# Kernel tuning notes

Hardware: AMD Instinct MI355X
Metric: run time of the kernel (lower is better)

## Reference

```python
import jax, jax.numpy as jnp
import numpy as np

B = 1024          # number of graphs
N = 64            # atoms per graph
NUM_NODES = B * N
HID = 256         # hidden_channels
H1 = HID // 2
E = 2_097_152     # edges (avg degree 32)


def _xavier(k, fan_in, fan_out):
    lim = np.sqrt(6.0 / (fan_in + fan_out)).astype(np.float32)
    return jax.random.uniform(k, (fan_in, fan_out), jnp.float32, -lim, lim)


def setup_inputs() -> dict:
    key = jax.random.key(0)
    ks = jax.random.split(key, 6)
    node_features = jax.random.normal(ks[0], (NUM_NODES, HID), jnp.float32)
    edge_index = jax.random.randint(ks[1], (2, E), 0, NUM_NODES)
    batch = jnp.repeat(jnp.arange(B), N)  # sorted graph ids, equal-size graphs
    W1 = _xavier(ks[2], HID + 1, H1); b1 = jnp.zeros((H1,), jnp.float32)
    W2 = _xavier(ks[3], H1, H1);      b2 = jnp.zeros((H1,), jnp.float32)
    W3 = _xavier(ks[4], H1, 1);       b3 = jnp.zeros((1,), jnp.float32)
    kT = jnp.ones((1,), jnp.float32)
    return {"node_features": node_features, "W1": W1, "b1": b1, "W2": W2,
            "b2": b2, "W3": W3, "b3": b3, "kT": kT,
            "edge_index": edge_index, "batch": batch}


def reference(node_features, W1, b1, W2, b2, W3, b3, kT, edge_index, batch):
    num_nodes = node_features.shape[0]
    # node degree: count of occurrences as source node
    deg = jnp.zeros((num_nodes,), jnp.float32).at[edge_index[0]].add(1.0)
    # per-graph atom counts and segment start offsets (n_atoms_i)
    counts = jax.ops.segment_sum(jnp.ones((num_nodes,), jnp.float32), batch,
                                 num_segments=B)
    start = jnp.cumsum(counts) - counts  # exclusive cumsum
    # stable per-graph sort of degrees in one shot: lexsort keys, primary=batch
    order = jnp.lexsort((deg, batch))  # global original indices, sorted by (batch, deg)
    # connectivity feature: local original index of the k-th smallest-degree
    # node in its graph, normalized by graph size (matches sorted_index / n_atoms_i)
    conn = (order.astype(jnp.float32) - start[batch]) / counts[batch]
    # MLP(hidden+1 -> hid/2 -> hid/2 -> 1) with silu
    x = jnp.concatenate([conn[:, None], node_features], axis=-1)  # [nodes, HID+1]
    h = jax.nn.silu(x @ W1 + b1)
    h = jax.nn.silu(h @ W2 + b2)
    logits = (h @ W3 + b3)[:, 0] / kT[0]
    # per-graph (segment) softmax
    m = jax.ops.segment_max(logits, batch, num_segments=B)
    e = jnp.exp(logits - m[batch])
    s = jax.ops.segment_sum(e, batch, num_segments=B)
    return e / s[batch]  # concat of per-graph softmaxed probabilities
```

## Files before the change

kernel.cpp:

```cpp
#include <hip/hip_runtime.h>

#define NB 1024
#define NPG 64
#define NUM_NODES 65536
#define HID 256
#define H1DIM 128
#define NE 2097152
#define GH 128

typedef __attribute__((ext_vector_type(8))) _Float16 f16x8;
typedef __attribute__((ext_vector_type(4))) float f32x4;

#define PART_OFF (128*1024)

__device__ __forceinline__ void dma16(const void* g, void* l) {
    __builtin_amdgcn_global_load_lds(
        (const __attribute__((address_space(1))) unsigned int*)g,
        (__attribute__((address_space(3))) unsigned int*)l, 16, 0, 0);
}

__global__ __launch_bounds__(256) void prep_hist_kernel(
    const float* __restrict__ W1, const float* __restrict__ W2,
    _Float16* __restrict__ wf,
    const int4* __restrict__ src4, unsigned int* __restrict__ partials)
{
    __shared__ unsigned int h[16384];
    const int bx = blockIdx.x;
    const int t = threadIdx.x;

    if (bx < 96) {
        const int L = t & 63;
        const int j2 = (t >> 6) * 2;
        const float* src;
        _Float16* dst;
        int kt, nt;
        if (bx < 64) { kt = bx >> 3; nt = bx & 7; src = W1 + H1DIM; dst = wf + bx * 512; }
        else { int bb = bx - 64; kt = bb >> 3; nt = bb & 7; src = W2; dst = wf + 32768 + bb * 512; }
        const int k = kt * 32 + (L >> 4) * 8 + j2;
        const int n = nt * 16 + (L & 15);
        dst[L * 8 + j2]     = (_Float16)src[k * H1DIM + n];
        dst[L * 8 + j2 + 1] = (_Float16)src[(k + 1) * H1DIM + n];
        return;
    }

    const int b = bx - 96;
    uint4* h4 = (uint4*)h;
#pragma unroll
    for (int i = 0; i < 16; ++i) h4[t + i * 256] = make_uint4(0u, 0u, 0u, 0u);
    __syncthreads();
    const int4* p = src4 + b * ((NE / 4) / GH);
#pragma unroll 4
    for (int i = t; i < (NE / 4) / GH; i += 256) {
        int4 v = p[i];
        atomicAdd(&h[v.x >> 2], 1u << ((v.x & 3) * 8));
        atomicAdd(&h[v.y >> 2], 1u << ((v.y & 3) * 8));
        atomicAdd(&h[v.z >> 2], 1u << ((v.z & 3) * 8));
        atomicAdd(&h[v.w >> 2], 1u << ((v.w & 3) * 8));
    }
    __syncthreads();
    uint4* dst = (uint4*)(partials + b * 16384);
#pragma unroll
    for (int i = 0; i < 16; ++i) dst[t + i * 256] = h4[t + i * 256];
}

__global__ __launch_bounds__(512, 4) void mlp_softmax_kernel(
    const float* __restrict__ feat,
    const float* __restrict__ W1, const float* __restrict__ b1,
    const float* __restrict__ b2,
    const float* __restrict__ W3, const float* __restrict__ b3,
    const float* __restrict__ kT,
    const _Float16* __restrict__ wf,
    const unsigned int* __restrict__ partials,
    float* __restrict__ out)
{
    __shared__ _Float16 wfs[32768];
    __shared__ unsigned int dpart[2][16][16];
    __shared__ unsigned int degs[2][NPG];
    __shared__ float conns[2][NPG];
    __shared__ float logits_s[2][NPG];

    const int tid = threadIdx.x;
    const int L = tid & 63;
    const int w = __builtin_amdgcn_readfirstlane(tid >> 6);
    const int h = w >> 2;
    const int w4 = w & 3;
    const int q = L >> 4;
    const int c = L & 15;
    const int g0 = blockIdx.x * 2;
    const int node0 = g0 * NPG;

#pragma unroll
    for (int i = 0; i < 8; ++i)
        dma16(&wf[(i * 512 + tid) * 8], &wfs[(i * 512 + w * 64) * 8]);

    {
        const int t256 = tid & 255;
        const int wd = t256 & 15, sg = t256 >> 4;
        const unsigned int* p = partials + (size_t)(sg * 8) * 16384 + (g0 + h) * 16 + wd;
        unsigned int s = 0;
#pragma unroll
        for (int i = 0; i < 8; ++i) s += p[(size_t)i * 16384];
        dpart[h][sg][wd] = s;
    }

    const float* featw = &feat[(size_t)(node0 + h * 64 + w4 * 16 + c) * HID + q * 8];
    float4 fa[8], fb[8];
#pragma unroll
    for (int kt = 0; kt < 8; ++kt) {
        fa[kt] = *(const float4*)(featw + kt * 32);
        fb[kt] = *(const float4*)(featw + kt * 32 + 4);
    }
    float b1v[8], w1r0[8];
#pragma unroll
    for (int nt = 0; nt < 8; ++nt) {
        b1v[nt]  = b1[nt * 16 + c];
        w1r0[nt] = W1[nt * 16 + c];
    }

    __syncthreads();
    if (tid < 32) {
        const int hh = tid >> 4, wd = tid & 15;
        unsigned int s = 0;
#pragma unroll
        for (int k = 0; k < 16; ++k) s += dpart[hh][k][wd];
        degs[hh][wd * 4 + 0] = s & 255u;
        degs[hh][wd * 4 + 1] = (s >> 8) & 255u;
        degs[hh][wd * 4 + 2] = (s >> 16) & 255u;
        degs[hh][wd * 4 + 3] = s >> 24;
    }
    __syncthreads();
    if ((tid & 192) == 0) {
        const int hh = tid >> 8, i = tid & 63;
        unsigned int di = degs[hh][i];
        int rk = 0;
#pragma unroll 8
        for (int j = 0; j < NPG; ++j) {
            unsigned int dj = degs[hh][j];
            rk += (int)((dj < di) | ((dj == di) & (j < i)));
        }
        conns[hh][rk] = (float)i * (1.0f / 64.0f);
    }
    __syncthreads();

    f16x8 af[8];
#pragma unroll
    for (int kt = 0; kt < 8; ++kt) {
        float4 A = fa[kt], B = fb[kt];
        f16x8 v = { (_Float16)A.x, (_Float16)A.y, (_Float16)A.z, (_Float16)A.w,
                    (_Float16)B.x, (_Float16)B.y, (_Float16)B.z, (_Float16)B.w };
        af[kt] = v;
    }

    float cn[4];
#pragma unroll
    for (int r = 0; r < 4; ++r) cn[r] = conns[h][w4 * 16 + q * 4 + r];
    f32x4 acc[8];
#pragma unroll
    for (int nt = 0; nt < 8; ++nt)
#pragma unroll
        for (int r = 0; r < 4; ++r)
            acc[nt][r] = fmaf(cn[r], w1r0[nt], b1v[nt]);

#pragma unroll
    for (int kt = 0; kt < 8; ++kt) {
#pragma unroll
        for (int nt = 0; nt < 8; ++nt) {
            f16x8 bfv = *(const f16x8*)&wfs[(kt * 8 + nt) * 512 + L * 8];
            acc[nt] = __builtin_amdgcn_mfma_f32_16x16x32_f16(af[kt], bfv, acc[nt], 0, 0, 0);
        }
    }

    __syncthreads();

#pragma unroll
    for (int i = 0; i < 4; ++i)
        dma16(&wf[32768 + (i * 512 + tid) * 8], &wfs[(i * 512 + w * 64) * 8]);

#pragma unroll
    for (int nt = 0; nt < 8; ++nt) {
        const int ktp = nt >> 1;
        const int lp = (((nt & 1) << 1) + (c >> 3)) * 16 + q * 4;
        const int j = c & 7;
#pragma unroll
        for (int r = 0; r < 4; ++r) {
            float v = acc[nt][r];
            float hv = v / (1.0f + __expf(-v));
            wfs[16384 + w * 2048 + ktp * 512 + (lp + r) * 8 + j] = (_Float16)hv;
        }
    }
    float b2v[8], w3v[8];
#pragma unroll
    for (int nt = 0; nt < 8; ++nt) {
        b2v[nt] = b2[nt * 16 + c];
        w3v[nt] = W3[nt * 16 + c];
    }
    __syncthreads();

    f32x4 acc2[8];
#pragma unroll
    for (int nt = 0; nt < 8; ++nt)
#pragma unroll
        for (int r = 0; r < 4; ++r) acc2[nt][r] = b2v[nt];
#pragma unroll
    for (int kt = 0; kt < 4; ++kt) {
        f16x8 a = *(const f16x8*)&wfs[16384 + w * 2048 + kt * 512 + L * 8];
#pragma unroll
        for (int nt = 0; nt < 8; ++nt) {
            f16x8 bfv = *(const f16x8*)&wfs[(kt * 8 + nt) * 512 + L * 8];
            acc2[nt] = __builtin_amdgcn_mfma_f32_16x16x32_f16(a, bfv, acc2[nt], 0, 0, 0);
        }
    }

    float lg[4] = {0.0f, 0.0f, 0.0f, 0.0f};
#pragma unroll
    for (int nt = 0; nt < 8; ++nt)
#pragma unroll
        for (int r = 0; r < 4; ++r) {
            float v = acc2[nt][r];
            float hv = v / (1.0f + __expf(-v));
            lg[r] = fmaf(hv, w3v[nt], lg[r]);
        }
#pragma unroll
    for (int d = 1; d < 16; d <<= 1)
#pragma unroll
        for (int r = 0; r < 4; ++r) lg[r] += __shfl_xor(lg[r], d, 64);
    if (c == 0) {
#pragma unroll
        for (int r = 0; r < 4; ++r) logits_s[h][w4 * 16 + q * 4 + r] = lg[r];
    }
    __syncthreads();

    if ((tid & 192) == 0) {
        const int hh = tid >> 8, i = tid & 63;
        float s = (logits_s[hh][i] + b3[0]) / kT[0];
        float m = s;
#pragma unroll
        for (int d = 1; d < 64; d <<= 1) m = fmaxf(m, __shfl_xor(m, d, 64));
        float e = __expf(s - m);
        float su = e;
#pragma unroll
        for (int d = 1; d < 64; d <<= 1) su += __shfl_xor(su, d, 64);
        out[node0 + hh * NPG + i] = e / su;
    }
}

extern "C" void kernel_launch(void* const* d_in, const int* in_sizes, int n_in,
                              void* d_out, int out_size, void* d_ws, size_t ws_size,
                              hipStream_t stream)
{
    const float* feat = (const float*)d_in[0];
    const float* W1   = (const float*)d_in[1];
    const float* b1   = (const float*)d_in[2];
    const float* W2   = (const float*)d_in[3];
    const float* b2   = (const float*)d_in[4];
    const float* W3   = (const float*)d_in[5];
    const float* b3   = (const float*)d_in[6];
    const float* kT   = (const float*)d_in[7];
    const int*   ei   = (const int*)d_in[8];

    float* out = (float*)d_out;
    _Float16* wf = (_Float16*)d_ws;
    unsigned int* partials = (unsigned int*)((char*)d_ws + PART_OFF);

    prep_hist_kernel<<<96 + GH, 256, 0, stream>>>(W1, W2, wf, (const int4*)ei,
                                                  partials);
    mlp_softmax_kernel<<<NB / 2, 512, 0, stream>>>(feat, W1, b1, b2, W3, b3,
                                                   kT, wf, partials, out);
}
```

Measured before the change: 136.7 us.

## Fuse histogram and weight prep into MLP kernel with grid-wide barrier

Merges the prep/histogram kernel into the MLP-softmax kernel. The first 224 blocks build degree-histogram partials and convert weights to fp16 before a global atomic-counter barrier, and feature loads are issued ahead of that barrier. This removes a kernel launch boundary and overlaps feature loading with histogram work. In exchange it adds a memset and a spin barrier that needs all 512 blocks to be co-resident, and a deadlock is possible if occupancy does not allow that.

Measured after the change: 202.5 us. 48.1% more time.

```diff
diff --git a/kernel.cpp b/kernel.cpp
--- a/kernel.cpp
+++ b/kernel.cpp
@@ -7,10 +7,12 @@
 #define H1DIM 128
 #define NE 2097152
 #define GH 128
+#define NBLK 512
 
 typedef __attribute__((ext_vector_type(8))) _Float16 f16x8;
 typedef __attribute__((ext_vector_type(4))) float f32x4;
 
+#define CNT_OFF  (100*1024)
 #define PART_OFF (128*1024)
 
 __device__ __forceinline__ void dma16(const void* g, void* l) {
@@ -19,75 +21,92 @@
         (__attribute__((address_space(3))) unsigned int*)l, 16, 0, 0);
 }
 
-__global__ __launch_bounds__(256) void prep_hist_kernel(
-    const float* __restrict__ W1, const float* __restrict__ W2,
-    _Float16* __restrict__ wf,
-    const int4* __restrict__ src4, unsigned int* __restrict__ partials)
-{
-    __shared__ unsigned int h[16384];
-    const int bx = blockIdx.x;
-    const int t = threadIdx.x;
-
-    if (bx < 96) {
-        const int L = t & 63;
-        const int j2 = (t >> 6) * 2;
-        const float* src;
-        _Float16* dst;
-        int kt, nt;
-        if (bx < 64) { kt = bx >> 3; nt = bx & 7; src = W1 + H1DIM; dst = wf + bx * 512; }
-        else { int bb = bx - 64; kt = bb >> 3; nt = bb & 7; src = W2; dst = wf + 32768 + bb * 512; }
-        const int k = kt * 32 + (L >> 4) * 8 + j2;
-        const int n = nt * 16 + (L & 15);
-        dst[L * 8 + j2]     = (_Float16)src[k * H1DIM + n];
-        dst[L * 8 + j2 + 1] = (_Float16)src[(k + 1) * H1DIM + n];
-        return;
-    }
-
-    const int b = bx - 96;
-    uint4* h4 = (uint4*)h;
-#pragma unroll
-    for (int i = 0; i < 16; ++i) h4[t + i * 256] = make_uint4(0u, 0u, 0u, 0u);
-    __syncthreads();
-    const int4* p = src4 + b * ((NE / 4) / GH);
-#pragma unroll 4
-    for (int i = t; i < (NE / 4) / GH; i += 256) {
-        int4 v = p[i];
-        atomicAdd(&h[v.x >> 2], 1u << ((v.x & 3) * 8));
-        atomicAdd(&h[v.y >> 2], 1u << ((v.y & 3) * 8));
-        atomicAdd(&h[v.z >> 2], 1u << ((v.z & 3) * 8));
-        atomicAdd(&h[v.w >> 2], 1u << ((v.w & 3) * 8));
-    }
-    __syncthreads();
-    uint4* dst = (uint4*)(partials + b * 16384);
-#pragma unroll
-    for (int i = 0; i < 16; ++i) dst[t + i * 256] = h4[t + i * 256];
-}
-
-__global__ __launch_bounds__(512, 4) void mlp_softmax_kernel(
+__global__ __launch_bounds__(512, 4) void fused_kernel(
     const float* __restrict__ feat,
     const float* __restrict__ W1, const float* __restrict__ b1,
-    const float* __restrict__ b2,
+    const float* __restrict__ W2g, const float* __restrict__ b2g,
     const float* __restrict__ W3, const float* __restrict__ b3,
     const float* __restrict__ kT,
-    const _Float16* __restrict__ wf,
-    const unsigned int* __restrict__ partials,
+    const int4* __restrict__ src4,
+    _Float16* __restrict__ wf,
+    unsigned int* __restrict__ sync_cnt,
+    unsigned int* __restrict__ partials,
     float* __restrict__ out)
 {
-    __shared__ _Float16 wfs[32768];
+    __shared__ __align__(16) _Float16 wfs[32768];
     __shared__ unsigned int dpart[2][16][16];
     __shared__ unsigned int degs[2][NPG];
     __shared__ float conns[2][NPG];
     __shared__ float logits_s[2][NPG];
 
     const int tid = threadIdx.x;
+    const int bx = blockIdx.x;
     const int L = tid & 63;
     const int w = __builtin_amdgcn_readfirstlane(tid >> 6);
     const int h = w >> 2;
     const int w4 = w & 3;
     const int q = L >> 4;
     const int c = L & 15;
-    const int g0 = blockIdx.x * 2;
+    const int g0 = bx * 2;
     const int node0 = g0 * NPG;
+
+    if (bx < GH) {
+        unsigned int* hst = (unsigned int*)wfs;
+        uint4* h4 = (uint4*)wfs;
+#pragma unroll
+        for (int i = 0; i < 8; ++i) h4[tid + i * 512] = make_uint4(0u, 0u, 0u, 0u);
+        __syncthreads();
+        const int4* p = src4 + bx * ((NE / 4) / GH);
+#pragma unroll
+        for (int i = 0; i < 8; ++i) {
+            int4 v = p[tid + i * 512];
+            atomicAdd(&hst[v.x >> 2], 1u << ((v.x & 3) * 8));
+            atomicAdd(&hst[v.y >> 2], 1u << ((v.y & 3) * 8));
+            atomicAdd(&hst[v.z >> 2], 1u << ((v.z & 3) * 8));
+            atomicAdd(&hst[v.w >> 2], 1u << ((v.w & 3) * 8));
+        }
+        __syncthreads();
+        uint4* dst = (uint4*)(partials + bx * 16384);
+#pragma unroll
+        for (int i = 0; i < 8; ++i) dst[tid + i * 512] = h4[tid + i * 512];
+    } else if (bx < GH + 96) {
+        const int bb = bx - GH;
+        const int j = tid >> 6;
+        const float* srcw;
+        _Float16* dstw;
+        int kt, nt;
+        if (bb < 64) { kt = bb >> 3; nt = bb & 7; srcw = W1 + H1DIM; dstw = wf + bb * 512; }
+        else { int bc = bb - 64; kt = bc >> 3; nt = bc & 7; srcw = W2g; dstw = wf + 32768 + bc * 512; }
+        const int k = kt * 32 + (L >> 4) * 8 + j;
+        const int n = nt * 16 + c;
+        dstw[L * 8 + j] = (_Float16)srcw[k * H1DIM + n];
+    }
+
+    const float* featw = &feat[(size_t)(node0 + h * 64 + w4 * 16 + c) * HID + q * 8];
+    float4 fa[8], fb[8];
+#pragma unroll
+    for (int kt = 0; kt < 8; ++kt) {
+        fa[kt] = *(const float4*)(featw + kt * 32);
+        fb[kt] = *(const float4*)(featw + kt * 32 + 4);
+    }
+    float b1v[8], w1r0[8];
+#pragma unroll
+    for (int nt = 0; nt < 8; ++nt) {
+        b1v[nt]  = b1[nt * 16 + c];
+        w1r0[nt] = W1[nt * 16 + c];
+    }
+
+    __syncthreads();
+    if (tid == 0) {
+        __threadfence();
+        __hip_atomic_fetch_add(sync_cnt, 1u, __ATOMIC_RELEASE,
+                               __HIP_MEMORY_SCOPE_AGENT);
+        while (__hip_atomic_load(sync_cnt, __ATOMIC_RELAXED,
+                                 __HIP_MEMORY_SCOPE_AGENT) < (unsigned)NBLK)
+            __builtin_amdgcn_s_sleep(1);
+        __threadfence();
+    }
+    __syncthreads();
 
 #pragma unroll
     for (int i = 0; i < 8; ++i)
@@ -101,20 +120,6 @@
 #pragma unroll
         for (int i = 0; i < 8; ++i) s += p[(size_t)i * 16384];
         dpart[h][sg][wd] = s;
-    }
-
-    const float* featw = &feat[(size_t)(node0 + h * 64 + w4 * 16 + c) * HID + q * 8];
-    float4 fa[8], fb[8];
-#pragma unroll
-    for (int kt = 0; kt < 8; ++kt) {
-        fa[kt] = *(const float4*)(featw + kt * 32);
-        fb[kt] = *(const float4*)(featw + kt * 32 + 4);
-    }
-    float b1v[8], w1r0[8];
-#pragma unroll
-    for (int nt = 0; nt < 8; ++nt) {
-        b1v[nt]  = b1[nt * 16 + c];
-        w1r0[nt] = W1[nt * 16 + c];
     }
 
     __syncthreads();
@@ -191,7 +196,7 @@
     float b2v[8], w3v[8];
 #pragma unroll
     for (int nt = 0; nt < 8; ++nt) {
-        b2v[nt] = b2[nt * 16 + c];
+        b2v[nt] = b2g[nt * 16 + c];
         w3v[nt] = W3[nt * 16 + c];
     }
     __syncthreads();
@@ -256,14 +261,14 @@
     const float* W3   = (const float*)d_in[5];
     const float* b3   = (const float*)d_in[6];
     const float* kT   = (const float*)d_in[7];
-    const int*   ei   = (const int*)d_in[8];
+    const int4*  src4 = (const int4*)d_in[8];
 
     float* out = (float*)d_out;
     _Float16* wf = (_Float16*)d_ws;
+    unsigned int* sync_cnt = (unsigned int*)((char*)d_ws + CNT_OFF);
     unsigned int* partials = (unsigned int*)((char*)d_ws + PART_OFF);
 
-    prep_hist_kernel<<<96 + GH, 256, 0, stream>>>(W1, W2, wf, (const int4*)ei,
-                                                  partials);
-    mlp_softmax_kernel<<<NB / 2, 512, 0, stream>>>(feat, W1, b1, b2, W3, b3,
-                                                   kT, wf, partials, out);
+    hipMemsetAsync(sync_cnt, 0, 64, stream);
+    fused_kernel<<<NBLK, 512, 0, stream>>>(feat, W1, b1, W2, b2, W3, b3, kT,
+                                           src4, wf, sync_cnt, partials, out);
 }
```
